# Kernel optimization log

Hardware: AMD Instinct MI355X
Metric: run time of the kernel (lower is better)

Reference implementation:

```python
import jax, jax.numpy as jnp
import numpy as np

MARGIN = 0.5
CURV = 1.0
B, D = 8192, 128
N_CLASSES = 256


def setup_inputs() -> dict:
    key = jax.random.key(0)
    k1, k2, k3 = jax.random.split(key, 3)
    emb = jax.random.normal(k1, (B, D), dtype=jnp.float32)
    # project onto Poincare ball: random radii in (0, 0.8) so all norms < 1
    radii = 0.8 * jax.random.uniform(k2, (B, 1), dtype=jnp.float32)
    emb = emb / (jnp.linalg.norm(emb, axis=-1, keepdims=True) + 1e-6) * radii
    labels = jax.random.randint(k3, (B,), 0, N_CLASSES, dtype=jnp.int64)
    return {"embeddings": emb, "labels": labels}


def _poincare_dist_matrix(x, c):
    # d(x,y) = arccosh(1 + 2c||x-y||^2 / ((1-c||x||^2)(1-c||y||^2))) / sqrt(c)
    sq = jnp.sum(x * x, axis=-1)                       # (B,)
    gram = x @ x.T                                      # (B,B) GEMM
    d2 = jnp.maximum(sq[:, None] + sq[None, :] - 2.0 * gram, 0.0)
    denom = (1.0 - c * sq)[:, None] * (1.0 - c * sq)[None, :]
    arg = 1.0 + 2.0 * c * d2 / denom
    # clamp slightly above 1: arccosh grad is infinite at 1 (diagonal / identical pts)
    return jnp.arccosh(jnp.maximum(arg, 1.0 + 1e-7)) / jnp.sqrt(c)


def reference(embeddings, labels):
    dist = _poincare_dist_matrix(embeddings, CURV)      # (B,B)
    same = labels[:, None] == labels[None, :]
    eye = jnp.eye(labels.shape[0], dtype=bool)
    pos_mask = same & ~eye
    neg_mask = ~same
    has_pos = jnp.any(pos_mask, axis=1)
    has_neg = jnp.any(neg_mask, axis=1)
    valid = has_pos & has_neg
    d_pos = jnp.max(jnp.where(pos_mask, dist, -jnp.inf), axis=1)
    d_neg = jnp.min(jnp.where(neg_mask, dist, jnp.inf), axis=1)
    d_pos = jnp.where(has_pos, d_pos, 0.0)
    d_neg = jnp.where(has_neg, d_neg, 0.0)
    l = jnp.maximum(d_pos - d_neg + MARGIN, 0.0)
    l = jnp.where(valid, l, 0.0)
    cnt = jnp.sum(valid)
    return jnp.where(cnt > 0, jnp.sum(l) / jnp.maximum(cnt, 1), 0.0)
```

## Files before the change

### kernel.cpp

```cpp
#include <hip/hip_runtime.h>
#include <hip/hip_bf16.h>

typedef __attribute__((ext_vector_type(8))) __bf16 bf16x8;
typedef __attribute__((ext_vector_type(4))) float f32x4;
typedef unsigned short u16;

#define NB 8192
#define ND 128
#define NCHUNK 16
#define NEGINF (-__builtin_inff())
#define POSINF (__builtin_inff())

__device__ inline u16 f2b(float f){
  __hip_bfloat16 h = __float2bfloat16(f);
  return *reinterpret_cast<u16*>(&h);
}

extern "C" __global__ __launch_bounds__(256)
void prep_k(const float* __restrict__ x, const int* __restrict__ lab,
            u16* __restrict__ xb, float4* __restrict__ colp)
{
  const int tid = blockIdx.x * 256 + threadIdx.x;
  const int row = tid >> 5;
  const int sub = tid & 31;
  const float4 v = reinterpret_cast<const float4*>(x)[row * 32 + sub];
  float s = v.x*v.x + v.y*v.y + v.z*v.z + v.w*v.w;
  #pragma unroll
  for (int m = 1; m < 32; m <<= 1) s += __shfl_xor(s, m, 32);
  ushort4 o;
  o.x = f2b(v.x); o.y = f2b(v.y); o.z = f2b(v.z); o.w = f2b(v.w);
  reinterpret_cast<ushort4*>(xb)[row * 32 + sub] = o;
  if (sub == 0){
    const float p = 1.0f / (1.0f - s);
    colp[row] = make_float4(s, p, s * p, __int_as_float(lab[row]));
  }
}

extern "C" __global__ __launch_bounds__(256, 4)
void gram_k(const u16* __restrict__ xb, const float4* __restrict__ colp,
            float* __restrict__ ppos, float* __restrict__ pneg)
{
  __shared__ u16 Bt[128 * 128];
  const int wid  = threadIdx.x >> 6;
  const int lane = threadIdx.x & 63;
  const int m16  = lane & 15;
  const int quad = lane >> 4;
  const int R0  = blockIdx.x * 128;
  const int C0  = blockIdx.y * 512;
  const int WR0 = R0 + wid * 32;

  bf16x8 afrag[2][4];
  #pragma unroll
  for (int mt = 0; mt < 2; ++mt){
    const u16* arow = xb + (WR0 + mt*16 + m16) * ND;
    #pragma unroll
    for (int ks = 0; ks < 4; ++ks)
      afrag[mt][ks] = *reinterpret_cast<const bf16x8*>(arow + ks*32 + quad*8);
  }

  float sqi[8]; int labi[8];
  #pragma unroll
  for (int mt = 0; mt < 2; ++mt)
    #pragma unroll
    for (int r = 0; r < 4; ++r){
      const float4 cp = colp[WR0 + mt*16 + quad*4 + r];
      sqi[mt*4+r]  = cp.x;
      labi[mt*4+r] = __float_as_int(cp.w);
    }

  float vpos[8], vneg[8];
  #pragma unroll
  for (int i = 0; i < 8; ++i){ vpos[i] = NEGINF; vneg[i] = POSINF; }

  for (int ct = 0; ct < 4; ++ct){
    const int CT0 = C0 + ct * 128;
    __syncthreads();
    #pragma unroll
    for (int c = 0; c < 8; ++c){
      const int cc   = wid * 8 + c;
      const int brow = cc * 4 + quad;
      const int src  = m16 ^ (brow & 15);
      const u16* gsrc = xb + (CT0 + brow) * ND + src * 8;
      __builtin_amdgcn_global_load_lds(
          (__attribute__((address_space(1))) void*)gsrc,
          (__attribute__((address_space(3))) void*)(Bt + cc * 512), 16, 0, 0);
    }
    __syncthreads();

    #pragma unroll
    for (int half = 0; half < 2; ++half){
      f32x4 acc[2][4];
      #pragma unroll
      for (int mt = 0; mt < 2; ++mt)
        #pragma unroll
        for (int nt4 = 0; nt4 < 4; ++nt4){
          f32x4 z = {0.f, 0.f, 0.f, 0.f};
          acc[mt][nt4] = z;
        }

      #pragma unroll
      for (int ks = 0; ks < 4; ++ks){
        const int t = ks * 4 + quad;
        #pragma unroll
        for (int nt4 = 0; nt4 < 4; ++nt4){
          const int nt = half * 4 + nt4;
          const bf16x8 bfrag = *reinterpret_cast<const bf16x8*>(
              Bt + (nt*16 + m16) * 128 + ((t ^ m16) * 8));
          acc[0][nt4] = __builtin_amdgcn_mfma_f32_16x16x32_bf16(afrag[0][ks], bfrag, acc[0][nt4], 0, 0, 0);
          acc[1][nt4] = __builtin_amdgcn_mfma_f32_16x16x32_bf16(afrag[1][ks], bfrag, acc[1][nt4], 0, 0, 0);
        }
      }

      #pragma unroll
      for (int nt4 = 0; nt4 < 4; ++nt4){
        const int nt  = half * 4 + nt4;
        const float4 cp = colp[CT0 + nt*16 + m16];
        const float pj   = cp.y;
        const float spj  = cp.z;
        const int   labj = __float_as_int(cp.w);
        const float n2pj = -2.0f * pj;
        #pragma unroll
        for (int mt = 0; mt < 2; ++mt){
          const bool tilediag = (WR0 + mt*16) == (CT0 + nt*16);
          if (!tilediag){
            #pragma unroll
            for (int r = 0; r < 4; ++r){
              const int idx = mt*4 + r;
              const float u = fmaf(n2pj, acc[mt][nt4][r], fmaf(sqi[idx], pj, spj));
              const bool sm = (labi[idx] == labj);
              vpos[idx] = fmaxf(vpos[idx], sm ? u : NEGINF);
              vneg[idx] = fminf(vneg[idx], sm ? POSINF : u);
            }
          } else {
            #pragma unroll
            for (int r = 0; r < 4; ++r){
              const int idx = mt*4 + r;
              const float u = fmaf(n2pj, acc[mt][nt4][r], fmaf(sqi[idx], pj, spj));
              const bool sm = (labi[idx] == labj);
              const bool dg = (m16 == quad*4 + r);
              vpos[idx] = fmaxf(vpos[idx], (sm && !dg) ? u : NEGINF);
              vneg[idx] = fminf(vneg[idx], sm ? POSINF : u);
            }
          }
        }
      }
    }
  }

  #pragma unroll
  for (int i = 0; i < 8; ++i){
    #pragma unroll
    for (int m = 1; m < 16; m <<= 1){
      vpos[i] = fmaxf(vpos[i], __shfl_xor(vpos[i], m, 16));
      vneg[i] = fminf(vneg[i], __shfl_xor(vneg[i], m, 16));
    }
  }
  if (m16 == 0){
    #pragma unroll
    for (int i = 0; i < 8; ++i){
      const int row = WR0 + (i >> 2)*16 + quad*4 + (i & 3);
      ppos[blockIdx.y * NB + row] = vpos[i];
      pneg[blockIdx.y * NB + row] = vneg[i];
    }
  }
}

extern "C" __global__ __launch_bounds__(128)
void fin1_k(const float* __restrict__ ppos, const float* __restrict__ pneg,
            const float4* __restrict__ colp, float2* __restrict__ bpart)
{
  const int row = blockIdx.x * 128 + threadIdx.x;
  float up = NEGINF, un = POSINF;
  #pragma unroll
  for (int c = 0; c < NCHUNK; ++c){
    up = fmaxf(up, ppos[c * NB + row]);
    un = fminf(un, pneg[c * NB + row]);
  }
  const bool hp = (up > NEGINF);
  const bool hn = (un < POSINF);
  const float pi = colp[row].y;
  float dp = 0.0f, dn = 0.0f;
  if (hp){ float t = fmaxf(2.0f * up * pi, 1e-7f); dp = log1pf(t + sqrtf(t * (t + 2.0f))); }
  if (hn){ float t = fmaxf(2.0f * un * pi, 1e-7f); dn = log1pf(t + sqrtf(t * (t + 2.0f))); }
  float lsum = (hp && hn) ? fmaxf(dp - dn + 0.5f, 0.0f) : 0.0f;
  float lcnt = (hp && hn) ? 1.0f : 0.0f;
  #pragma unroll
  for (int m = 1; m < 64; m <<= 1){
    lsum += __shfl_xor(lsum, m, 64);
    lcnt += __shfl_xor(lcnt, m, 64);
  }
  __shared__ float2 s_p[2];
  if ((threadIdx.x & 63) == 0) s_p[threadIdx.x >> 6] = make_float2(lsum, lcnt);
  __syncthreads();
  if (threadIdx.x == 0){
    bpart[blockIdx.x] = make_float2(s_p[0].x + s_p[1].x, s_p[0].y + s_p[1].y);
  }
}

extern "C" __global__ __launch_bounds__(64)
void fin2_k(const float2* __restrict__ bpart, float* __restrict__ out)
{
  float2 p = bpart[threadIdx.x];
  float s = p.x, c = p.y;
  #pragma unroll
  for (int m = 1; m < 64; m <<= 1){
    s += __shfl_xor(s, m, 64);
    c += __shfl_xor(c, m, 64);
  }
  if (threadIdx.x == 0) out[0] = (c > 0.0f) ? (s / c) : 0.0f;
}

extern "C" void kernel_launch(void* const* d_in, const int* in_sizes, int n_in,
                              void* d_out, int out_size, void* d_ws, size_t ws_size,
                              hipStream_t stream)
{
  const float* x  = (const float*)d_in[0];
  const int* lab  = (const int*)d_in[1];
  char* ws = (char*)d_ws;
  u16*    xb   = (u16*)ws;
  float4* colp = (float4*)(ws + (size_t)2*1024*1024);
  float*  ppos = (float*)(ws + (size_t)2*1024*1024 + 128*1024);
  float*  pneg = (float*)(ws + (size_t)2*1024*1024 + 128*1024 + 512*1024);
  float2* bpart= (float2*)(ws + (size_t)2*1024*1024 + 128*1024 + 1024*1024);

  hipLaunchKernelGGL(prep_k, dim3(1024), dim3(256), 0, stream, x, lab, xb, colp);
  hipLaunchKernelGGL(gram_k, dim3(64, NCHUNK), dim3(256), 0, stream,
                     xb, colp, ppos, pneg);
  hipLaunchKernelGGL(fin1_k, dim3(64), dim3(128), 0, stream, ppos, pneg, colp, bpart);
  hipLaunchKernelGGL(fin2_k, dim3(1), dim3(64), 0, stream, bpart, (float*)d_out);
}
```

Baseline: 102.3 us.

## Exploit distance symmetry with upper-triangular tiles and atomic order-preserving reductions

Launches only the upper-triangular 128x128 tile pairs (2080 blocks) and, for each off-diagonal tile, reduces both row-wise and column-wise hardest positives and negatives, roughly halving the MFMA and epilogue work. Per-row partials now go through atomicMax and atomicMin on sign-flipped float encodings, initialised in prep_k, which replaces the 16-chunk partial buffers and their reduction in fin1_k. Each block now loads a single B tile up front. The cost is an extra column-direction epilogue, an LDS cross-wave reduction and global atomic contention, and the occupancy hint drops to 2 blocks per SIMD.

New measurement: 105.6 us. 1.03x slower.

```diff
diff --git a/kernel.cpp b/kernel.cpp
--- a/kernel.cpp
+++ b/kernel.cpp
@@ -4,21 +4,31 @@
 typedef __attribute__((ext_vector_type(8))) __bf16 bf16x8;
 typedef __attribute__((ext_vector_type(4))) float f32x4;
 typedef unsigned short u16;
+typedef unsigned int u32;
 
 #define NB 8192
 #define ND 128
-#define NCHUNK 16
 #define NEGINF (-__builtin_inff())
 #define POSINF (__builtin_inff())
+#define ENC_NEGINF 0x007FFFFFu
+#define ENC_POSINF 0xFF800000u
 
 __device__ inline u16 f2b(float f){
   __hip_bfloat16 h = __float2bfloat16(f);
   return *reinterpret_cast<u16*>(&h);
 }
+__device__ inline u32 encf(float f){
+  u32 b = __float_as_uint(f);
+  return b ^ (0x80000000u | (u32)(((int)b) >> 31));
+}
+__device__ inline float decf(u32 u){
+  return __uint_as_float(u ^ (0x80000000u | (u32)((~(int)u) >> 31)));
+}
 
 extern "C" __global__ __launch_bounds__(256)
 void prep_k(const float* __restrict__ x, const int* __restrict__ lab,
-            u16* __restrict__ xb, float4* __restrict__ colp)
+            u16* __restrict__ xb, float4* __restrict__ colp,
+            u32* __restrict__ ppos, u32* __restrict__ pneg)
 {
   const int tid = blockIdx.x * 256 + threadIdx.x;
   const int row = tid >> 5;
@@ -34,20 +44,39 @@
     const float p = 1.0f / (1.0f - s);
     colp[row] = make_float4(s, p, s * p, __int_as_float(lab[row]));
   }
-}
-
-extern "C" __global__ __launch_bounds__(256, 4)
+  if (sub == 1) ppos[row] = ENC_NEGINF;
+  if (sub == 2) pneg[row] = ENC_POSINF;
+}
+
+extern "C" __global__ __launch_bounds__(256, 2)
 void gram_k(const u16* __restrict__ xb, const float4* __restrict__ colp,
-            float* __restrict__ ppos, float* __restrict__ pneg)
+            u32* __restrict__ ppos, u32* __restrict__ pneg)
 {
   __shared__ u16 Bt[128 * 128];
   const int wid  = threadIdx.x >> 6;
   const int lane = threadIdx.x & 63;
   const int m16  = lane & 15;
   const int quad = lane >> 4;
-  const int R0  = blockIdx.x * 128;
-  const int C0  = blockIdx.y * 512;
-  const int WR0 = R0 + wid * 32;
+
+  int idx = (int)blockIdx.x;
+  int bi = (int)((129.0f - sqrtf((float)(16641 - 8 * idx))) * 0.5f);
+  while ((bi + 1) * (129 - (bi + 1)) / 2 <= idx) ++bi;
+  while (bi * (129 - bi) / 2 > idx) --bi;
+  const int bj = bi + (idx - bi * (129 - bi) / 2);
+  const bool diag = (bi == bj);
+  const int C0  = bj * 128;
+  const int WR0 = bi * 128 + wid * 32;
+
+  #pragma unroll
+  for (int c = 0; c < 8; ++c){
+    const int cc   = wid * 8 + c;
+    const int brow = cc * 4 + quad;
+    const int src  = m16 ^ (brow & 15);
+    const u16* gsrc = xb + (C0 + brow) * ND + src * 8;
+    __builtin_amdgcn_global_load_lds(
+        (const __attribute__((address_space(1))) void*)gsrc,
+        (__attribute__((address_space(3))) void*)(Bt + cc * 512), 16, 0, 0);
+  }
 
   bf16x8 afrag[2][4];
   #pragma unroll
@@ -58,92 +87,91 @@
       afrag[mt][ks] = *reinterpret_cast<const bf16x8*>(arow + ks*32 + quad*8);
   }
 
-  float sqi[8]; int labi[8];
+  float sqi[8], pi[8]; int labi[8];
   #pragma unroll
   for (int mt = 0; mt < 2; ++mt)
     #pragma unroll
     for (int r = 0; r < 4; ++r){
       const float4 cp = colp[WR0 + mt*16 + quad*4 + r];
       sqi[mt*4+r]  = cp.x;
+      pi[mt*4+r]   = cp.y;
       labi[mt*4+r] = __float_as_int(cp.w);
     }
 
-  float vpos[8], vneg[8];
-  #pragma unroll
-  for (int i = 0; i < 8; ++i){ vpos[i] = NEGINF; vneg[i] = POSINF; }
-
-  for (int ct = 0; ct < 4; ++ct){
-    const int CT0 = C0 + ct * 128;
-    __syncthreads();
-    #pragma unroll
-    for (int c = 0; c < 8; ++c){
-      const int cc   = wid * 8 + c;
-      const int brow = cc * 4 + quad;
-      const int src  = m16 ^ (brow & 15);
-      const u16* gsrc = xb + (CT0 + brow) * ND + src * 8;
-      __builtin_amdgcn_global_load_lds(
-          (__attribute__((address_space(1))) void*)gsrc,
-          (__attribute__((address_space(3))) void*)(Bt + cc * 512), 16, 0, 0);
-    }
-    __syncthreads();
-
-    #pragma unroll
-    for (int half = 0; half < 2; ++half){
-      f32x4 acc[2][4];
+  __syncthreads();
+
+  f32x4 acc[2][8];
+  #pragma unroll
+  for (int mt = 0; mt < 2; ++mt)
+    #pragma unroll
+    for (int nt = 0; nt < 8; ++nt){
+      f32x4 z = {0.f, 0.f, 0.f, 0.f};
+      acc[mt][nt] = z;
+    }
+
+  #pragma unroll
+  for (int ks = 0; ks < 4; ++ks){
+    const int t = ks * 4 + quad;
+    #pragma unroll
+    for (int nt = 0; nt < 8; ++nt){
+      const bf16x8 bfrag = *reinterpret_cast<const bf16x8*>(
+          Bt + (nt*16 + m16) * 128 + ((t ^ m16) * 8));
+      acc[0][nt] = __builtin_amdgcn_mfma_f32_16x16x32_bf16(afrag[0][ks], bfrag, acc[0][nt], 0, 0, 0);
+      acc[1][nt] = __builtin_amdgcn_mfma_f32_16x16x32_bf16(afrag[1][ks], bfrag, acc[1][nt], 0, 0, 0);
+    }
+  }
+
+  float vpos[8], vneg[8], cpos[8], cneg[8];
+  #pragma unroll
+  for (int i = 0; i < 8; ++i){
+    vpos[i] = NEGINF; vneg[i] = POSINF;
+    cpos[i] = NEGINF; cneg[i] = POSINF;
+  }
+
+  if (!diag){
+    #pragma unroll
+    for (int nt = 0; nt < 8; ++nt){
+      const float4 cp = colp[C0 + nt*16 + m16];
+      const float sqj  = cp.x;
+      const float pj   = cp.y;
+      const int   labj = __float_as_int(cp.w);
       #pragma unroll
       for (int mt = 0; mt < 2; ++mt)
         #pragma unroll
-        for (int nt4 = 0; nt4 < 4; ++nt4){
-          f32x4 z = {0.f, 0.f, 0.f, 0.f};
-          acc[mt][nt4] = z;
+        for (int r = 0; r < 4; ++r){
+          const int i = mt*4 + r;
+          const float d2 = fmaf(-2.0f, acc[mt][nt][r], sqi[i] + sqj);
+          const float ur = d2 * pj;
+          const float uc = d2 * pi[i];
+          const bool sm = (labi[i] == labj);
+          vpos[i]  = fmaxf(vpos[i],  sm ? ur : NEGINF);
+          vneg[i]  = fminf(vneg[i],  sm ? POSINF : ur);
+          cpos[nt] = fmaxf(cpos[nt], sm ? uc : NEGINF);
+          cneg[nt] = fminf(cneg[nt], sm ? POSINF : uc);
         }
-
-      #pragma unroll
-      for (int ks = 0; ks < 4; ++ks){
-        const int t = ks * 4 + quad;
+    }
+  } else {
+    #pragma unroll
+    for (int nt = 0; nt < 8; ++nt){
+      const float4 cp = colp[C0 + nt*16 + m16];
+      const float sqj  = cp.x;
+      const float pj   = cp.y;
+      const int   labj = __float_as_int(cp.w);
+      const int colin  = nt*16 + m16;
+      #pragma unroll
+      for (int mt = 0; mt < 2; ++mt)
         #pragma unroll
-        for (int nt4 = 0; nt4 < 4; ++nt4){
-          const int nt = half * 4 + nt4;
-          const bf16x8 bfrag = *reinterpret_cast<const bf16x8*>(
-              Bt + (nt*16 + m16) * 128 + ((t ^ m16) * 8));
-          acc[0][nt4] = __builtin_amdgcn_mfma_f32_16x16x32_bf16(afrag[0][ks], bfrag, acc[0][nt4], 0, 0, 0);
-          acc[1][nt4] = __builtin_amdgcn_mfma_f32_16x16x32_bf16(afrag[1][ks], bfrag, acc[1][nt4], 0, 0, 0);
+        for (int r = 0; r < 4; ++r){
+          const int i = mt*4 + r;
+          const float d2 = fmaf(-2.0f, acc[mt][nt][r], sqi[i] + sqj);
+          const float ur = d2 * pj;
+          const bool sm = (labi[i] == labj);
+          const bool dg = (colin == wid*32 + mt*16 + quad*4 + r);
+          float ep = sm ? ur : NEGINF;
+          ep = dg ? NEGINF : ep;
+          vpos[i] = fmaxf(vpos[i], ep);
+          vneg[i] = fminf(vneg[i], sm ? POSINF : ur);
         }
-      }
-
-      #pragma unroll
-      for (int nt4 = 0; nt4 < 4; ++nt4){
-        const int nt  = half * 4 + nt4;
-        const float4 cp = colp[CT0 + nt*16 + m16];
-        const float pj   = cp.y;
-        const float spj  = cp.z;
-        const int   labj = __float_as_int(cp.w);
-        const float n2pj = -2.0f * pj;
-        #pragma unroll
-        for (int mt = 0; mt < 2; ++mt){
-          const bool tilediag = (WR0 + mt*16) == (CT0 + nt*16);
-          if (!tilediag){
-            #pragma unroll
-            for (int r = 0; r < 4; ++r){
-              const int idx = mt*4 + r;
-              const float u = fmaf(n2pj, acc[mt][nt4][r], fmaf(sqi[idx], pj, spj));
-              const bool sm = (labi[idx] == labj);
-              vpos[idx] = fmaxf(vpos[idx], sm ? u : NEGINF);
-              vneg[idx] = fminf(vneg[idx], sm ? POSINF : u);
-            }
-          } else {
-            #pragma unroll
-            for (int r = 0; r < 4; ++r){
-              const int idx = mt*4 + r;
-              const float u = fmaf(n2pj, acc[mt][nt4][r], fmaf(sqi[idx], pj, spj));
-              const bool sm = (labi[idx] == labj);
-              const bool dg = (m16 == quad*4 + r);
-              vpos[idx] = fmaxf(vpos[idx], (sm && !dg) ? u : NEGINF);
-              vneg[idx] = fminf(vneg[idx], sm ? POSINF : u);
-            }
-          }
-        }
-      }
     }
   }
 
@@ -159,29 +187,57 @@
     #pragma unroll
     for (int i = 0; i < 8; ++i){
       const int row = WR0 + (i >> 2)*16 + quad*4 + (i & 3);
-      ppos[blockIdx.y * NB + row] = vpos[i];
-      pneg[blockIdx.y * NB + row] = vneg[i];
+      atomicMax(ppos + row, encf(vpos[i]));
+      atomicMin(pneg + row, encf(vneg[i]));
+    }
+  }
+
+  if (!diag){
+    #pragma unroll
+    for (int nt = 0; nt < 8; ++nt){
+      cpos[nt] = fmaxf(cpos[nt], __shfl_xor(cpos[nt], 16));
+      cpos[nt] = fmaxf(cpos[nt], __shfl_xor(cpos[nt], 32));
+      cneg[nt] = fminf(cneg[nt], __shfl_xor(cneg[nt], 16));
+      cneg[nt] = fminf(cneg[nt], __shfl_xor(cneg[nt], 32));
+    }
+    float* cbP = reinterpret_cast<float*>(Bt);
+    float* cbN = cbP + 512;
+    __syncthreads();
+    if (quad == 0){
+      #pragma unroll
+      for (int nt = 0; nt < 8; ++nt){
+        cbP[wid*128 + nt*16 + m16] = cpos[nt];
+        cbN[wid*128 + nt*16 + m16] = cneg[nt];
+      }
+    }
+    __syncthreads();
+    if (threadIdx.x < 128){
+      const int c = threadIdx.x;
+      float P = NEGINF, N = POSINF;
+      #pragma unroll
+      for (int w = 0; w < 4; ++w){
+        P = fmaxf(P, cbP[w*128 + c]);
+        N = fminf(N, cbN[w*128 + c]);
+      }
+      atomicMax(ppos + C0 + c, encf(P));
+      atomicMin(pneg + C0 + c, encf(N));
     }
   }
 }
 
 extern "C" __global__ __launch_bounds__(128)
-void fin1_k(const float* __restrict__ ppos, const float* __restrict__ pneg,
+void fin1_k(const u32* __restrict__ ppos, const u32* __restrict__ pneg,
             const float4* __restrict__ colp, float2* __restrict__ bpart)
 {
   const int row = blockIdx.x * 128 + threadIdx.x;
-  float up = NEGINF, un = POSINF;
-  #pragma unroll
-  for (int c = 0; c < NCHUNK; ++c){
-    up = fmaxf(up, ppos[c * NB + row]);
-    un = fminf(un, pneg[c * NB + row]);
-  }
+  const float up = decf(ppos[row]);
+  const float un = decf(pneg[row]);
   const bool hp = (up > NEGINF);
   const bool hn = (un < POSINF);
-  const float pi = colp[row].y;
+  const float pr = colp[row].y;
   float dp = 0.0f, dn = 0.0f;
-  if (hp){ float t = fmaxf(2.0f * up * pi, 1e-7f); dp = log1pf(t + sqrtf(t * (t + 2.0f))); }
-  if (hn){ float t = fmaxf(2.0f * un * pi, 1e-7f); dn = log1pf(t + sqrtf(t * (t + 2.0f))); }
+  if (hp){ float t = fmaxf(2.0f * up * pr, 1e-7f); dp = log1pf(t + sqrtf(t * (t + 2.0f))); }
+  if (hn){ float t = fmaxf(2.0f * un * pr, 1e-7f); dn = log1pf(t + sqrtf(t * (t + 2.0f))); }
   float lsum = (hp && hn) ? fmaxf(dp - dn + 0.5f, 0.0f) : 0.0f;
   float lcnt = (hp && hn) ? 1.0f : 0.0f;
   #pragma unroll
@@ -192,9 +248,8 @@
   __shared__ float2 s_p[2];
   if ((threadIdx.x & 63) == 0) s_p[threadIdx.x >> 6] = make_float2(lsum, lcnt);
   __syncthreads();
-  if (threadIdx.x == 0){
+  if (threadIdx.x == 0)
     bpart[blockIdx.x] = make_float2(s_p[0].x + s_p[1].x, s_p[0].y + s_p[1].y);
-  }
 }
 
 extern "C" __global__ __launch_bounds__(64)
@@ -219,13 +274,12 @@
   char* ws = (char*)d_ws;
   u16*    xb   = (u16*)ws;
   float4* colp = (float4*)(ws + (size_t)2*1024*1024);
-  float*  ppos = (float*)(ws + (size_t)2*1024*1024 + 128*1024);
-  float*  pneg = (float*)(ws + (size_t)2*1024*1024 + 128*1024 + 512*1024);
-  float2* bpart= (float2*)(ws + (size_t)2*1024*1024 + 128*1024 + 1024*1024);
-
-  hipLaunchKernelGGL(prep_k, dim3(1024), dim3(256), 0, stream, x, lab, xb, colp);
-  hipLaunchKernelGGL(gram_k, dim3(64, NCHUNK), dim3(256), 0, stream,
-                     xb, colp, ppos, pneg);
+  u32*    ppos = (u32*)(ws + (size_t)2*1024*1024 + 128*1024);
+  u32*    pneg = (u32*)(ws + (size_t)2*1024*1024 + 160*1024);
+  float2* bpart= (float2*)(ws + (size_t)2*1024*1024 + 192*1024);
+
+  hipLaunchKernelGGL(prep_k, dim3(1024), dim3(256), 0, stream, x, lab, xb, colp, ppos, pneg);
+  hipLaunchKernelGGL(gram_k, dim3(2080), dim3(256), 0, stream, xb, colp, ppos, pneg);
   hipLaunchKernelGGL(fin1_k, dim3(64), dim3(128), 0, stream, ppos, pneg, colp, bpart);
   hipLaunchKernelGGL(fin2_k, dim3(1), dim3(64), 0, stream, bpart, (float*)d_out);
 }
```
